# Kernel tuning notes

Hardware: AMD Instinct MI355X
Metric: run time of the kernel (lower is better)

## Reference

```python
import jax, jax.numpy as jnp
import numpy as np

B, T, C = 4, 2048, 1024
H = 16
HD = C // H  # 64


def setup_inputs() -> dict:
    key = jax.random.key(0)
    ks = jax.random.split(key, 4)
    x = jax.random.normal(ks[0], (B, T, C), dtype=jnp.float32)
    # c_attn: Linear(C, 3C, bias=False)  (qkv_bias=False)
    w_attn = jax.random.normal(ks[1], (C, 3 * C), dtype=jnp.float32) / np.sqrt(C)
    # c_proj: Linear(C, C) with bias (nn.Linear default)
    w_proj = jax.random.normal(ks[2], (C, C), dtype=jnp.float32) / np.sqrt(C)
    b_proj = jax.random.normal(ks[3], (C,), dtype=jnp.float32) * 0.01
    return {"x": x, "w_attn": w_attn, "w_proj": w_proj, "b_proj": b_proj}


def reference(x, w_attn, w_proj, b_proj):
    b, t, c = x.shape
    qkv = x @ w_attn  # [B,T,3C]
    q, k, v = jnp.split(qkv, 3, axis=-1)
    # [B,H,T,HD]
    q = q.reshape(b, t, H, HD).transpose(0, 2, 1, 3)
    k = k.reshape(b, t, H, HD).transpose(0, 2, 1, 3)
    v = v.reshape(b, t, H, HD).transpose(0, 2, 1, 3)
    scale = 1.0 / np.sqrt(HD)
    attn = jnp.einsum('bhqd,bhkd->bhqk', q, k) * scale  # [B,H,T,T]
    causal = jnp.tril(jnp.ones((t, t), dtype=bool))
    attn = jnp.where(causal, attn, -jnp.inf)
    attn = jax.nn.softmax(attn, axis=-1)
    out = jnp.einsum('bhqk,bhkd->bhqd', attn, v)  # [B,H,T,HD]
    out = out.transpose(0, 2, 1, 3).reshape(b, t, c)
    return out @ w_proj + b_proj
```

## Files before the change

### kernel.cpp

```cpp
#include <hip/hip_runtime.h>

#define BB 4
#define TT 2048
#define CC 1024
#define C3 3072
#define HH 16
#define HD 64
#define BT 8192

#define TS 32
#define TSZ (64 * TS)

typedef __bf16 bf16x8 __attribute__((ext_vector_type(8)));
typedef float floatx4 __attribute__((ext_vector_type(4)));
typedef unsigned uintx2 __attribute__((ext_vector_type(2)));
typedef unsigned short u16;

__device__ __forceinline__ u16 f2bf(float f) {
  union { float f; unsigned u; } a; a.f = f;
  return (u16)((a.u + 0x7fffu + ((a.u >> 16) & 1u)) >> 16);
}
__device__ __forceinline__ bf16x8 ld8(const u16* p) { return *(const bf16x8*)p; }
__device__ __forceinline__ floatx4 mfma16(bf16x8 a, bf16x8 b, floatx4 c) {
  return __builtin_amdgcn_mfma_f32_16x16x32_bf16(a, b, c, 0, 0, 0);
}

__device__ __forceinline__ void gload16(const u16* g, u16* l) {
  __builtin_amdgcn_global_load_lds(
      (const __attribute__((address_space(1))) void*)g,
      (__attribute__((address_space(3))) void*)l, 16, 0, 0);
}

__device__ __forceinline__ void qd_xchg(unsigned a, unsigned b,
                                        unsigned& r0, unsigned& r1) {
  uintx2 t = __builtin_amdgcn_permlane32_swap(a, b, false, false);
  uintx2 r = __builtin_amdgcn_permlane16_swap(t[0], t[1], false, false);
  r0 = r[0]; r1 = r[1];
}

#define BARR do { asm volatile("" ::: "memory"); \
                  __builtin_amdgcn_s_barrier(); \
                  asm volatile("" ::: "memory"); } while (0)
#define VMW4 asm volatile("s_waitcnt vmcnt(4)" ::: "memory")
#define VMW0 asm volatile("s_waitcnt vmcnt(0)" ::: "memory")

__global__ __launch_bounds__(256) void prep_kernel(
    const float4* __restrict__ x4, ushort4* __restrict__ xb4,
    const float* __restrict__ w_attn, u16* __restrict__ waT,
    const float* __restrict__ w_proj, u16* __restrict__ wpT) {
  __shared__ float s[64][65];
  const int t = threadIdx.x;
  const int bid = blockIdx.x;

  if (bid < 8192) {
    const int i = bid * 256 + t;
    float4 v = x4[i];
    ushort4 o; o.x = f2bf(v.x); o.y = f2bf(v.y); o.z = f2bf(v.z); o.w = f2bf(v.w);
    xb4[i] = o;
    return;
  }

  const float* src; u16* dst; int N, bx, by;
  if (bid < 8960) { const int b2 = bid - 8192; src = w_attn; dst = waT; N = C3;
                    bx = b2 % 48; by = b2 / 48; }
  else            { const int b2 = bid - 8960; src = w_proj; dst = wpT; N = CC;
                    bx = b2 % 16; by = b2 / 16; }
  const int K = CC;
  const int r = t >> 4;
  const int c = (t & 15) * 4;
  const int k0 = by * 64, n0 = bx * 64;
#pragma unroll
  for (int i = 0; i < 4; ++i) {
    float4 v = *(const float4*)&src[(size_t)(k0 + r + i * 16) * N + n0 + c];
    s[r + i * 16][c + 0] = v.x; s[r + i * 16][c + 1] = v.y;
    s[r + i * 16][c + 2] = v.z; s[r + i * 16][c + 3] = v.w;
  }
  __syncthreads();
#pragma unroll
  for (int i = 0; i < 4; ++i) {
    const int nn = r + i * 16;
    ushort4 o;
    o.x = f2bf(s[c + 0][nn]); o.y = f2bf(s[c + 1][nn]);
    o.z = f2bf(s[c + 2][nn]); o.w = f2bf(s[c + 3][nn]);
    *(ushort4*)&dst[(size_t)(n0 + nn) * K + k0 + c] = o;
  }
}

template<int MODE>
__global__ __launch_bounds__(512, 2) void gemm256_kernel(
    const u16* __restrict__ A, const u16* __restrict__ B,
    const float* __restrict__ bias, float* __restrict__ outf,
    u16* __restrict__ qk, u16* __restrict__ vT, int N, int K) {
  __shared__ u16 lds[2][24576];

  const int t = threadIdx.x;
  const int lane = t & 63, lr = lane & 15, qd = lane >> 4;
  const int w = t >> 6, wm = w >> 1, wn = w & 1;
  const int m0 = blockIdx.y * 256, n0 = blockIdx.x * 128;

  const int srow = t >> 3;
  const int scol = ((t & 7) ^ (srow & 7)) * 8;
  const u16* Asrc = A + (size_t)(m0 + srow) * K + scol;
  const u16* Bsrc = B + (size_t)(n0 + srow) * K + scol;
  const int wvb = (t & ~63) * 8;

  const int NT = K >> 6;
  floatx4 acc[4][4] = {};

  const int abase = (wm * 64 + lr) * 64;
  const int bbase = (wn * 64 + lr) * 64;
  const int csw0 = (qd * 8) ^ ((lr & 7) * 8);
  const int csw1 = (32 + qd * 8) ^ ((lr & 7) * 8);

#define STG_A(PR, QA, TK) do { if ((TK) < NT) \
    gload16(Asrc + (size_t)((QA) * 64) * K + (TK) * 64, \
            &lds[PR][(QA) * 4096 + wvb]); } while (0)
#define STG_B(PR, HB, TK) do { if ((TK) < NT) \
    gload16(Bsrc + (size_t)((HB) * 64) * K + (TK) * 64, \
            &lds[PR][16384 + (HB) * 4096 + wvb]); } while (0)

  bf16x8 af[4][2], bf[2][2];
#define READ_A(PR) do { _Pragma("unroll") for (int mi = 0; mi < 4; ++mi) { \
    const u16* p_ = &lds[PR][mi * 1024 + abase]; \
    af[mi][0] = ld8(p_ + csw0); af[mi][1] = ld8(p_ + csw1); } } while (0)
#define READ_B(PR, NJ0) do { _Pragma("unroll") for (int nj = 0; nj < 2; ++nj) { \
    const u16* p_ = &lds[PR][16384 + ((NJ0) + nj) * 1024 + bbase]; \
    bf[nj][0] = ld8(p_ + csw0); bf[nj][1] = ld8(p_ + csw1); } } while (0)
#define MFMA16(NJ0) do { __builtin_amdgcn_s_setprio(1); _Pragma("unroll") \
    for (int mi = 0; mi < 4; ++mi) _Pragma("unroll") for (int nj = 0; nj < 2; ++nj) { \
      acc[mi][(NJ0) + nj] = mfma16(af[mi][0], bf[nj][0], acc[mi][(NJ0) + nj]); \
      acc[mi][(NJ0) + nj] = mfma16(af[mi][1], bf[nj][1], acc[mi][(NJ0) + nj]); } \
    __builtin_amdgcn_s_setprio(0); } while (0)

  STG_A(0, 0, 0); STG_A(0, 1, 0); STG_A(0, 2, 0); STG_A(0, 3, 0);
  STG_B(0, 0, 0); STG_B(0, 1, 0);
  STG_A(1, 0, 1); STG_A(1, 1, 1); STG_A(1, 2, 1); STG_A(1, 3, 1);
  VMW4; BARR;

  const int NITER = NT >> 1;
  for (int it = 0; it < NITER; ++it) {
    const int T1 = 2 * it + 1, T2 = 2 * it + 2, T3 = 2 * it + 3;
    const bool last = (it == NITER - 1);
    STG_B(1, 0, T1); STG_B(1, 1, T1);
    READ_A(0); READ_B(0, 0); MFMA16(0);
    BARR;
    STG_A(0, 0, T2); STG_A(0, 1, T2); STG_A(0, 2, T2); STG_A(0, 3, T2);
    READ_B(0, 2); MFMA16(2);
    if (last) { VMW0; } else { VMW4; }
    BARR;
    STG_B(0, 0, T2); STG_B(0, 1, T2);
    READ_A(1); READ_B(1, 0); MFMA16(0);
    BARR;
    STG_A(1, 0, T3); STG_A(1, 1, T3); STG_A(1, 2, T3); STG_A(1, 3, T3);
    READ_B(1, 2); MFMA16(2);
    if (last) { VMW0; } else { VMW4; }
    BARR;
  }
#undef STG_A
#undef STG_B
#undef READ_A
#undef READ_B
#undef MFMA16

  u16* flat = &lds[0][0];
  if constexpr (MODE == 2) {
    const int rowg0 = m0 + wm * 64;
    const int colg0 = n0 + wn * 64;
#pragma unroll
    for (int nj = 0; nj < 4; ++nj) {
      const int col = colg0 + nj * 16 + lr;
      const float bv = bias[col];
#pragma unroll
      for (int mi = 0; mi < 4; ++mi)
#pragma unroll
        for (int i = 0; i < 4; ++i)
          outf[(size_t)(rowg0 + mi * 16 + qd * 4 + i) * N + col] = acc[mi][nj][i] + bv;
    }
  } else {
    const bool isV = (n0 >= 2 * CC);
    if (!isV) {
      const float qs = (n0 < CC) ? 0.18033688011f : 1.0f;
      u16* Tw = flat + w * (32 * 72);
      const int C0 = n0 + wn * 64;
#pragma unroll
      for (int mi2 = 0; mi2 < 2; ++mi2) {
#pragma unroll
        for (int mh = 0; mh < 2; ++mh)
#pragma unroll
          for (int nj = 0; nj < 4; ++nj)
#pragma unroll
            for (int i = 0; i < 4; ++i)
              Tw[(mh * 16 + qd * 4 + i) * 72 + nj * 16 + lr] =
                  f2bf(acc[mi2 * 2 + mh][nj][i] * qs);
        const int R0 = m0 + wm * 64 + mi2 * 32;
#pragma unroll
        for (int s = 0; s < 4; ++s) {
          const int rl = s * 8 + (lane >> 3);
          const int c0 = (lane & 7) * 8;
          *(bf16x8*)&qk[(size_t)(R0 + rl) * (2 * CC) + C0 + c0] =
              ld8(&Tw[rl * 72 + c0]);
        }
      }
    } else {
      u16* Tv = flat + w * (64 * 72);
      const int bI = m0 >> 11;
      const int tbase = (m0 & (TT - 1)) + wm * 64;
      const int dim0 = (n0 - 2 * CC) + wn * 64;
#pragma unroll
      for (int nj = 0; nj < 4; ++nj)
#pragma unroll
        for (int mi = 0; mi < 4; ++mi)
#pragma unroll
          for (int i = 0; i < 4; ++i)
            Tv[(nj * 16 + lr) * 72 + mi * 16 + qd * 4 + i] =
                f2bf(acc[mi][nj][i]);
#pragma unroll
      for (int s = 0; s < 8; ++s) {
        const int dl = s * 8 + (lane >> 3);
        const int t0 = (lane & 7) * 8;
        *(bf16x8*)&vT[((size_t)(bI << 10) + dim0 + dl) * TT + tbase + t0] =
            ld8(&Tv[dl * 72 + t0]);
      }
    }
  }
}

__global__ __launch_bounds__(256) void gemm_kernel(
    const u16* __restrict__ A, const u16* __restrict__ B,
    const float* __restrict__ bias, float* __restrict__ outf,
    int M, int N, int K) {
  __shared__ u16 smem[2][2][2 * TSZ];

  const int t = threadIdx.x;
  const int w = t >> 6, lane = t & 63, lr = lane & 15, qd = lane >> 4;
  const int wm = w >> 1, wn = w & 1;
  const int m0 = blockIdx.y * 128, n0 = blockIdx.x * 128;

  const int sr = t >> 2;
  const int sc = (t & 3) * 8;
  const int wb = (t & ~63) * 8;
  const u16* Ag = A + (size_t)(m0 + sr) * K + sc;
  const u16* Bg = B + (size_t)(n0 + sr) * K + sc;

  floatx4 acc[4][4] = {};

  {
    u16* sA = &smem[0][0][0];
    u16* sB = &smem[0][1][0];
    gload16(Ag,                  &sA[wb]);
    gload16(Ag + (size_t)64 * K, &sA[TSZ + wb]);
    gload16(Bg,                  &sB[wb]);
    gload16(Bg + (size_t)64 * K, &sB[TSZ + wb]);
  }
  __syncthreads();

  for (int k0 = 0; k0 < K; k0 += 32) {
    const int p = (k0 >> 5) & 1;
    if (k0 + 32 < K) {
      u16* sA = &smem[p ^ 1][0][0];
      u16* sB = &smem[p ^ 1][1][0];
      gload16(Ag + k0 + 32,                  &sA[wb]);
      gload16(Ag + (size_t)64 * K + k0 + 32, &sA[TSZ + wb]);
      gload16(Bg + k0 + 32,                  &sB[wb]);
      gload16(Bg + (size_t)64 * K + k0 + 32, &sB[TSZ + wb]);
    }
    const u16* sA = &smem[p][0][0];
    const u16* sB = &smem[p][1][0];

    bf16x8 af[4], bf[4];
#pragma unroll
    for (int mj = 0; mj < 4; ++mj) af[mj] = ld8(&sA[(wm * 64 + mj * 16 + lr) * TS + qd * 8]);
#pragma unroll
    for (int nj = 0; nj < 4; ++nj) bf[nj] = ld8(&sB[(wn * 64 + nj * 16 + lr) * TS + qd * 8]);
#pragma unroll
    for (int mj = 0; mj < 4; ++mj)
#pragma unroll
      for (int nj = 0; nj < 4; ++nj)
        acc[mj][nj] = mfma16(af[mj], bf[nj], acc[mj][nj]);
    __syncthreads();
  }

  const int rowg0 = m0 + wm * 64;
  const int colg0 = n0 + wn * 64;
#pragma unroll
  for (int nj = 0; nj < 4; ++nj) {
    const int col = colg0 + nj * 16 + lr;
    const float bv = bias[col];
#pragma unroll
    for (int mj = 0; mj < 4; ++mj)
#pragma unroll
      for (int i = 0; i < 4; ++i)
        outf[(size_t)(rowg0 + mj * 16 + qd * 4 + i) * N + col] = acc[mj][nj][i] + bv;
  }
}

__global__ __launch_bounds__(256, 5) void attn_kernel(const u16* __restrict__ qk,
                                                      const u16* __restrict__ vT,
                                                      u16* __restrict__ att) {
  __shared__ u16 sKV[2][4][TSZ];

  const int t = threadIdx.x;
  const int w = t >> 6, lane = t & 63, lr = lane & 15, qd = lane >> 4;
  const int qtile = 31 - blockIdx.y;
  const int bh = blockIdx.x;
  const int b = bh >> 4, h = bh & 15;
  const int q0 = qtile * 64;
  const u16* qbase = qk + (size_t)b * TT * (2 * CC);

  const u16* qp = qbase + (size_t)(q0 + w * 16 + lr) * (2 * CC) + h * HD;
  const bf16x8 qf0 = ld8(qp + qd * 8);
  const bf16x8 qf1 = ld8(qp + 32 + qd * 8);

  const int sr = t >> 2, sc = (t & 3) * 8;
  const int wb = (t & ~63) * 8;
  const u16* Kg = qbase + (size_t)sr * (2 * CC) + CC + h * HD + sc;
  const u16* Vg = vT + ((size_t)bh * HD + sr) * TT + sc;

  float lsum = 0.f;
  floatx4 o[4] = {};
  const int myq = q0 + w * 16 + lr;

  {
    u16* b0 = &sKV[0][0][0];
    gload16(Kg,      &b0[wb]);
    gload16(Kg + 32, &b0[TSZ + wb]);
    gload16(Vg,      &b0[2 * TSZ + wb]);
    gload16(Vg + 32, &b0[3 * TSZ + wb]);
  }
  __syncthreads();

  for (int kt = 0; kt <= qtile; ++kt) {
    if (kt < qtile) {
      const int kn = (kt + 1) * 64;
      u16* bn = &sKV[(kt + 1) & 1][0][0];
      gload16(Kg + (size_t)kn * (2 * CC),      &bn[wb]);
      gload16(Kg + (size_t)kn * (2 * CC) + 32, &bn[TSZ + wb]);
      gload16(Vg + kn,                         &bn[2 * TSZ + wb]);
      gload16(Vg + kn + 32,                    &bn[3 * TSZ + wb]);
    }

    const u16* sK0 = &sKV[kt & 1][0][0];
    const u16* sK1 = &sKV[kt & 1][1][0];
    const u16* sV0 = &sKV[kt & 1][2][0];
    const u16* sV1 = &sKV[kt & 1][3][0];

    floatx4 s[4] = {};
#pragma unroll
    for (int j = 0; j < 4; ++j) {
      bf16x8 kf0 = ld8(&sK0[(j * 16 + lr) * TS + qd * 8]);
      bf16x8 kf1 = ld8(&sK1[(j * 16 + lr) * TS + qd * 8]);
      s[j] = mfma16(kf0, qf0, s[j]);
      s[j] = mfma16(kf1, qf1, s[j]);
    }

    const bool diag = (kt == qtile);
    unsigned W[4][2];
#pragma unroll
    for (int j = 0; j < 4; ++j) {
      float p[4];
#pragma unroll
      for (int i = 0; i < 4; ++i) {
        p[i] = __builtin_amdgcn_exp2f(s[j][i]);
        if (diag) {
          const int key = kt * 64 + j * 16 + qd * 4 + i;
          p[i] = (key <= myq) ? p[i] : 0.f;
        }
        lsum += p[i];
      }
      W[j][0] = __builtin_amdgcn_perm(__float_as_uint(p[1]), __float_as_uint(p[0]), 0x07060302);
      W[j][1] = __builtin_amdgcn_perm(__float_as_uint(p[3]), __float_as_uint(p[2]), 0x07060302);
    }

    uint4 F0, F1;
    qd_xchg(W[0][0], W[1][0], F0.x, F0.z);
    qd_xchg(W[0][1], W[1][1], F0.y, F0.w);
    qd_xchg(W[2][0], W[3][0], F1.x, F1.z);
    qd_xchg(W[2][1], W[3][1], F1.y, F1.w);
    const bf16x8 pf0 = __builtin_bit_cast(bf16x8, F0);
    const bf16x8 pf1 = __builtin_bit_cast(bf16x8, F1);

#pragma unroll
    for (int j = 0; j < 4; ++j) {
      bf16x8 vf0 = ld8(&sV0[(j * 16 + lr) * TS + qd * 8]);
      bf16x8 vf1 = ld8(&sV1[(j * 16 + lr) * TS + qd * 8]);
      o[j] = mfma16(pf0, vf0, o[j]);
      o[j] = mfma16(pf1, vf1, o[j]);
    }
    __syncthreads();
  }

  lsum += __shfl_xor(lsum, 16);
  lsum += __shfl_xor(lsum, 32);
  float linv[4];
#pragma unroll
  for (int i = 0; i < 4; ++i) linv[i] = 1.0f / __shfl(lsum, qd * 4 + i);

#pragma unroll
  for (int j = 0; j < 4; ++j)
#pragma unroll
    for (int i = 0; i < 4; ++i) {
      const size_t row = (size_t)b * TT + q0 + w * 16 + qd * 4 + i;
      att[row * CC + h * HD + j * 16 + lr] = f2bf(o[j][i] * linv[i]);
    }
}

extern "C" void kernel_launch(void* const* d_in, const int* in_sizes, int n_in,
                              void* d_out, int out_size, void* d_ws, size_t ws_size,
                              hipStream_t stream) {
  const float* x      = (const float*)d_in[0];
  const float* w_attn = (const float*)d_in[1];
  const float* w_proj = (const float*)d_in[2];
  const float* b_proj = (const float*)d_in[3];
  float* out = (float*)d_out;

  char* ws = (char*)d_ws;
  u16* xb  = (u16*)(ws + 0);
  u16* waT = (u16*)(ws + 16777216);
  u16* wpT = (u16*)(ws + 23068672);
  u16* qk  = (u16*)(ws + 25165824);
  u16* vT  = (u16*)(ws + 58720256);
  u16* att = (u16*)(ws + 75497472);

  prep_kernel<<<9216, 256, 0, stream>>>((const float4*)x, (ushort4*)xb,
                                        w_attn, waT, w_proj, wpT);

  gemm256_kernel<1><<<dim3(24, 32), 512, 0, stream>>>(xb, waT, nullptr, nullptr,
                                                      qk, vT, C3, CC);

  attn_kernel<<<dim3(64, 32), 256, 0, stream>>>(qk, vT, att);

  gemm_kernel<<<dim3(8, 64), 256, 0, stream>>>(att, wpT, b_proj, out,
                                               BT, CC, CC);
}
```

Before: 226.9 us.

## Use 128-query attention tiles with 8 waves sharing K/V and XOR-swizzled LDS

The attention kernel now runs 512-thread blocks that each cover 128 queries instead of 64, so every K/V tile loaded into shared memory is reused by twice as many waves and global K/V traffic drops. The shared-memory layout becomes full 64-wide rows with an XOR swizzle on the column index, meant to avoid bank conflicts. Waves in the lower half of a block skip compute on the final key tile but still hit the barrier, so some compute sits idle on the diagonal. Occupancy per block changes, and the grid halves in the query dimension.

Measured after the change: 236.8 us. +4.4%, slower.

```diff
diff --git a/kernel.cpp b/kernel.cpp
--- a/kernel.cpp
+++ b/kernel.cpp
@@ -294,97 +294,99 @@
   }
 }
 
-__global__ __launch_bounds__(256, 5) void attn_kernel(const u16* __restrict__ qk,
+__global__ __launch_bounds__(512, 4) void attn_kernel(const u16* __restrict__ qk,
                                                       const u16* __restrict__ vT,
                                                       u16* __restrict__ att) {
-  __shared__ u16 sKV[2][4][TSZ];
+  __shared__ u16 sKV[2][2][4096];
 
   const int t = threadIdx.x;
   const int w = t >> 6, lane = t & 63, lr = lane & 15, qd = lane >> 4;
-  const int qtile = 31 - blockIdx.y;
+  const int qt = 15 - blockIdx.y;
   const int bh = blockIdx.x;
   const int b = bh >> 4, h = bh & 15;
-  const int q0 = qtile * 64;
+  const int q0 = qt * 128;
   const u16* qbase = qk + (size_t)b * TT * (2 * CC);
 
   const u16* qp = qbase + (size_t)(q0 + w * 16 + lr) * (2 * CC) + h * HD;
   const bf16x8 qf0 = ld8(qp + qd * 8);
   const bf16x8 qf1 = ld8(qp + 32 + qd * 8);
 
-  const int sr = t >> 2, sc = (t & 3) * 8;
-  const int wb = (t & ~63) * 8;
+  const int sr = t >> 3;
+  const int sc = ((t & 7) ^ (sr & 7)) * 8;
+  const int wvb = (t & ~63) * 8;
   const u16* Kg = qbase + (size_t)sr * (2 * CC) + CC + h * HD + sc;
   const u16* Vg = vT + ((size_t)bh * HD + sr) * TT + sc;
 
   float lsum = 0.f;
   floatx4 o[4] = {};
   const int myq = q0 + w * 16 + lr;
+  const int dtile = 2 * qt + (w >> 2);
+  const int ktmax = 2 * qt + 1;
 
   {
     u16* b0 = &sKV[0][0][0];
-    gload16(Kg,      &b0[wb]);
-    gload16(Kg + 32, &b0[TSZ + wb]);
-    gload16(Vg,      &b0[2 * TSZ + wb]);
-    gload16(Vg + 32, &b0[3 * TSZ + wb]);
+    gload16(Kg, &b0[wvb]);
+    gload16(Vg, &b0[4096 + wvb]);
   }
   __syncthreads();
 
-  for (int kt = 0; kt <= qtile; ++kt) {
-    if (kt < qtile) {
+  const int cs0 = (qd * 8) ^ ((lr & 7) * 8);
+  const int cs1 = (32 + qd * 8) ^ ((lr & 7) * 8);
+
+  for (int kt = 0; kt <= ktmax; ++kt) {
+    if (kt < ktmax) {
       const int kn = (kt + 1) * 64;
       u16* bn = &sKV[(kt + 1) & 1][0][0];
-      gload16(Kg + (size_t)kn * (2 * CC),      &bn[wb]);
-      gload16(Kg + (size_t)kn * (2 * CC) + 32, &bn[TSZ + wb]);
-      gload16(Vg + kn,                         &bn[2 * TSZ + wb]);
-      gload16(Vg + kn + 32,                    &bn[3 * TSZ + wb]);
-    }
-
-    const u16* sK0 = &sKV[kt & 1][0][0];
-    const u16* sK1 = &sKV[kt & 1][1][0];
-    const u16* sV0 = &sKV[kt & 1][2][0];
-    const u16* sV1 = &sKV[kt & 1][3][0];
-
-    floatx4 s[4] = {};
-#pragma unroll
-    for (int j = 0; j < 4; ++j) {
-      bf16x8 kf0 = ld8(&sK0[(j * 16 + lr) * TS + qd * 8]);
-      bf16x8 kf1 = ld8(&sK1[(j * 16 + lr) * TS + qd * 8]);
-      s[j] = mfma16(kf0, qf0, s[j]);
-      s[j] = mfma16(kf1, qf1, s[j]);
-    }
-
-    const bool diag = (kt == qtile);
-    unsigned W[4][2];
-#pragma unroll
-    for (int j = 0; j < 4; ++j) {
-      float p[4];
-#pragma unroll
-      for (int i = 0; i < 4; ++i) {
-        p[i] = __builtin_amdgcn_exp2f(s[j][i]);
-        if (diag) {
-          const int key = kt * 64 + j * 16 + qd * 4 + i;
-          p[i] = (key <= myq) ? p[i] : 0.f;
+      gload16(Kg + (size_t)kn * (2 * CC), &bn[wvb]);
+      gload16(Vg + kn,                    &bn[4096 + wvb]);
+    }
+
+    if (kt <= dtile) {
+      const u16* sK = &sKV[kt & 1][0][0];
+      const u16* sV = &sKV[kt & 1][1][0];
+
+      floatx4 s[4] = {};
+#pragma unroll
+      for (int j = 0; j < 4; ++j) {
+        bf16x8 kf0 = ld8(&sK[(j * 16 + lr) * 64 + cs0]);
+        bf16x8 kf1 = ld8(&sK[(j * 16 + lr) * 64 + cs1]);
+        s[j] = mfma16(kf0, qf0, s[j]);
+        s[j] = mfma16(kf1, qf1, s[j]);
+      }
+
+      const bool diag = (kt == dtile);
+      unsigned W[4][2];
+#pragma unroll
+      for (int j = 0; j < 4; ++j) {
+        float p[4];
+#pragma unroll
+        for (int i = 0; i < 4; ++i) {
+          p[i] = __builtin_amdgcn_exp2f(s[j][i]);
+          if (diag) {
+            const int key = kt * 64 + j * 16 + qd * 4 + i;
+            p[i] = (key <= myq) ? p[i] : 0.f;
+          }
+          lsum += p[i];
         }
-        lsum += p[i];
+        W[j][0] = __builtin_amdgcn_perm(__float_as_uint(p[1]), __float_as_uint(p[0]), 0x07060302);
+        W[j][1] = __builtin_amdgcn_perm(__float_as_uint(p[3]), __float_as_uint(p[2]), 0x07060302);
       }
-      W[j][0] = __builtin_amdgcn_perm(__float_as_uint(p[1]), __float_as_uint(p[0]), 0x07060302);
-      W[j][1] = __builtin_amdgcn_perm(__float_as_uint(p[3]), __float_as_uint(p[2]), 0x07060302);
-    }
-
-    uint4 F0, F1;
-    qd_xchg(W[0][0], W[1][0], F0.x, F0.z);
-    qd_xchg(W[0][1], W[1][1], F0.y, F0.w);
-    qd_xchg(W[2][0], W[3][0], F1.x, F1.z);
-    qd_xchg(W[2][1], W[3][1], F1.y, F1.w);
-    const bf16x8 pf0 = __builtin_bit_cast(bf16x8, F0);
-    const bf16x8 pf1 = __builtin_bit_cast(bf16x8, F1);
-
-#pragma unroll
-    for (int j = 0; j < 4; ++j) {
-      bf16x8 vf0 = ld8(&sV0[(j * 16 + lr) * TS + qd * 8]);
-      bf16x8 vf1 = ld8(&sV1[(j * 16 + lr) * TS + qd * 8]);
-      o[j] = mfma16(pf0, vf0, o[j]);
-      o[j] = mfma16(pf1, vf1, o[j]);
+
+      uint4 F0, F1;
+      qd_xchg(W[0][0], W[1][0], F0.x, F0.z);
+      qd_xchg(W[0][1], W[1][1], F0.y, F0.w);
+      qd_xchg(W[2][0], W[3][0], F1.x, F1.z);
+      qd_xchg(W[2][1], W[3][1], F1.y, F1.w);
+      const bf16x8 pf0 = __builtin_bit_cast(bf16x8, F0);
+      const bf16x8 pf1 = __builtin_bit_cast(bf16x8, F1);
+
+#pragma unroll
+      for (int j = 0; j < 4; ++j) {
+        bf16x8 vf0 = ld8(&sV[(j * 16 + lr) * 64 + cs0]);
+        bf16x8 vf1 = ld8(&sV[(j * 16 + lr) * 64 + cs1]);
+        o[j] = mfma16(pf0, vf0, o[j]);
+        o[j] = mfma16(pf1, vf1, o[j]);
+      }
     }
     __syncthreads();
   }
@@ -427,7 +429,7 @@
   gemm256_kernel<1><<<dim3(24, 32), 512, 0, stream>>>(xb, waT, nullptr, nullptr,
                                                       qk, vT, C3, CC);
 
-  attn_kernel<<<dim3(64, 32), 256, 0, stream>>>(qk, vT, att);
+  attn_kernel<<<dim3(64, 16), 512, 0, stream>>>(qk, vT, att);
 
   gemm_kernel<<<dim3(8, 64), 256, 0, stream>>>(att, wpT, b_proj, out,
                                                BT, CC, CC);
```
